# Performance work log

Measured on AMD Instinct MI355X. Metric: run time of the kernel, lower is better.

## Reference

```python
import jax, jax.numpy as jnp
import numpy as np

N = 100000   # num nodes
E = 1600000  # num edges
F = 64       # node_feature_dim
H = 128      # hidden_dim
G = 64       # num graphs in batch
L = 3        # num_gnn_layers


def setup_inputs() -> dict:
    key = jax.random.key(0)
    ks = jax.random.split(key, 24)
    s = 0.05
    nrm = lambda k, shape: jax.random.normal(k, shape, jnp.float32) * s
    return dict(
        node_features=jax.random.normal(ks[0], (N, F), jnp.float32),
        edge_index=jax.random.randint(ks[1], (2, E), 0, N, dtype=jnp.int32),
        batch=jnp.sort(jax.random.randint(ks[2], (N,), 0, G, dtype=jnp.int32)),
        enc_w1=nrm(ks[3], (F, H)), enc_b1=jnp.zeros((H,), jnp.float32),
        enc_w2=nrm(ks[4], (H, H)), enc_b2=jnp.zeros((H,), jnp.float32),
        gcn_w=nrm(ks[5], (L, H, H)), gcn_b=jnp.zeros((L, H), jnp.float32),
        dec_w1=nrm(ks[6], (2 * H, H)), dec_b1=jnp.zeros((H,), jnp.float32),
        dec_w2=nrm(ks[7], (H, 64)), dec_b2=jnp.zeros((64,), jnp.float32),
        dec_w3=nrm(ks[8], (64, 3)), dec_b3=jnp.zeros((3,), jnp.float32),
        val_w1=nrm(ks[9], (2 * H, H)), val_b1=jnp.zeros((H,), jnp.float32),
        val_w2=nrm(ks[10], (H, 1)), val_b2=jnp.zeros((1,), jnp.float32),
    )


def _forward(node_features, edge_index, batch,
             enc_w1, enc_b1, enc_w2, enc_b2, gcn_w, gcn_b,
             dec_w1, dec_b1, dec_w2, dec_b2, dec_w3, dec_b3,
             val_w1, val_b1, val_w2, val_b2):
    n = node_features.shape[0]
    # node encoder (dropout is identity in eval)
    x = jax.nn.relu(node_features @ enc_w1 + enc_b1)
    x = x @ enc_w2 + enc_b2

    # GCN normalization with self-loops (PyG gcn_norm)
    loops = jnp.arange(n, dtype=edge_index.dtype)
    src = jnp.concatenate([edge_index[0], loops])
    dst = jnp.concatenate([edge_index[1], loops])
    deg = jax.ops.segment_sum(jnp.ones_like(src, jnp.float32), dst, num_segments=n)
    dinv = jax.lax.rsqrt(deg)  # deg >= 1 due to self-loops
    norm = (dinv[src] * dinv[dst])[:, None]  # [E+N, 1]

    for l in range(gcn_w.shape[0]):
        xw = x @ gcn_w[l]                      # [N, H]
        msg = xw[src] * norm                   # gather + scale
        agg = jax.ops.segment_sum(msg, dst, num_segments=n) + gcn_b[l]
        x = x + jax.nn.relu(agg)               # residual

    # global pools per graph
    graph_sum = jax.ops.segment_sum(x, batch, num_segments=G)
    counts = jax.ops.segment_sum(jnp.ones((n, 1), x.dtype), batch, num_segments=G)
    graph_mean = graph_sum / jnp.maximum(counts, 1.0)
    graph_max = jax.ops.segment_max(x, batch, num_segments=G)
    graph_repr = jnp.concatenate([graph_mean, graph_max], axis=1)  # [G, 2H]

    h = jax.nn.relu(graph_repr @ dec_w1 + dec_b1)
    h = jax.nn.relu(h @ dec_w2 + dec_b2)
    logits = h @ dec_w3 + dec_b3               # [G, 3]

    adaptation_prob = jax.nn.sigmoid(logits[:, 0])
    layer_priorities = jax.nn.softmax(logits[:, 1:2], axis=-1)
    urgency_score = jax.nn.sigmoid(logits[:, 2])

    v = jax.nn.relu(graph_repr @ val_w1 + val_b1)
    value_estimate = v @ val_w2 + val_b2       # [G, 1]
    return adaptation_prob, layer_priorities, urgency_score, value_estimate


def reference(node_features, edge_index, batch,
              enc_w1, enc_b1, enc_w2, enc_b2, gcn_w, gcn_b,
              dec_w1, dec_b1, dec_w2, dec_b2, dec_w3, dec_b3,
              val_w1, val_b1, val_w2, val_b2):
    return _forward(node_features, edge_index, batch,
                    enc_w1, enc_b1, enc_w2, enc_b2, gcn_w, gcn_b,
                    dec_w1, dec_b1, dec_w2, dec_b2, dec_w3, dec_b3,
                    val_w1, val_b1, val_w2, val_b2)
```

## Files before the change

### kernel.cpp

```cpp
#include <hip/hip_runtime.h>
#include <math.h>

constexpr int HD = 128;
constexpr int FD = 64;
constexpr int PCH = 32;
constexpr int BKT_SHIFT = 8;
constexpr int EPB = 2048;
constexpr float FP8_SCALE = 16.f;
constexpr float FP8_INV_SCALE = 1.f / 16.f;

typedef unsigned int uint;
typedef unsigned short ushort;
typedef unsigned char uchar;

using bf16x8 = __attribute__((ext_vector_type(8))) short;
using f32x4  = __attribute__((ext_vector_type(4))) float;

#if defined(__has_builtin)
#if __has_builtin(__builtin_amdgcn_cvt_pk_f32_fp8) && __has_builtin(__builtin_amdgcn_cvt_pk_fp8_f32)
#define HW_FP8 1
#endif
#endif

static __device__ inline ushort f2bf(float f) {
  uint u = __float_as_uint(f);
  return (ushort)((u + 0x7fffu + ((u >> 16) & 1u)) >> 16);
}
static __device__ inline float bf2f(ushort b) {
  return __uint_as_float((uint)b << 16);
}
static __device__ inline uint pack2bf(float a, float b) {
  return (uint)f2bf(a) | ((uint)f2bf(b) << 16);
}

static __device__ inline uchar enc_fp8_byte(float f) {
#ifdef HW_FP8
  return (uchar)(__builtin_amdgcn_cvt_pk_fp8_f32(f, f, 0, false) & 0xff);
#else
  float a = fabsf(f);
  uint s = (f < 0.f) ? 0x80u : 0u;
  if (!(a > 0.f)) return (uchar)s;
  a = fminf(a, 448.f);
  uint b = __float_as_uint(a);
  int e = (int)(b >> 23) - 127;
  if (e < -6) {
    int q = (int)rintf(a * 512.f);
    if (q <= 0) return (uchar)s;
    if (q >= 8) return (uchar)(s | 0x08u);
    return (uchar)(s | (uint)q);
  }
  uint r = b + 0x7ffffu + ((b >> 20) & 1u);
  uint m = (r >> 20) & 7u;
  int ee = (int)(r >> 23) - 127 + 7;
  if (ee <= 0) return (uchar)(s | 0x08u);
  if (ee > 15) return (uchar)(s | 0x7eu);
  return (uchar)(s | ((uint)ee << 3) | m);
#endif
}

static __device__ inline float dec_fp8_byte(uint em_s) {
  uint s = (em_s & 0x80u) << 24;
  uint em = em_s & 0x7fu;
  float v;
  if (em < 8) v = (float)em * (1.f / 512.f);
  else v = __uint_as_float((em + (120u << 3)) << 20);
  return __uint_as_float(__float_as_uint(v) | s);
}

static __device__ inline void dec_fp8x4(uint u, float* dst) {
#ifdef HW_FP8
  auto a = __builtin_amdgcn_cvt_pk_f32_fp8((int)u, false);
  auto b = __builtin_amdgcn_cvt_pk_f32_fp8((int)u, true);
  dst[0] = a[0]; dst[1] = a[1]; dst[2] = b[0]; dst[3] = b[1];
#else
  dst[0] = dec_fp8_byte(u & 0xffu);
  dst[1] = dec_fp8_byte((u >> 8) & 0xffu);
  dst[2] = dec_fp8_byte((u >> 16) & 0xffu);
  dst[3] = dec_fp8_byte(u >> 24);
#endif
}

__global__ void zero_int_kernel(int* __restrict__ p, int n) {
  int i = blockIdx.x * blockDim.x + threadIdx.x;
  if (i < n) p[i] = 0;
}

__global__ __launch_bounds__(256) void bucket_count_kernel(const int* __restrict__ dst,
    int* __restrict__ bucket_count, int e, int nbk) {
  __shared__ int hist[512];
  int t = threadIdx.x;
  for (int i = t; i < nbk; i += 256) hist[i] = 0;
  __syncthreads();
  int lo = blockIdx.x * EPB;
  int hi = lo + EPB; if (hi > e) hi = e;
  for (int i = lo + t; i < hi; i += 256) atomicAdd(&hist[dst[i] >> BKT_SHIFT], 1);
  __syncthreads();
  for (int i = t; i < nbk; i += 256) {
    int c = hist[i];
    if (c) atomicAdd(&bucket_count[i], c);
  }
}

__global__ __launch_bounds__(512) void bucket_scan_kernel(const int* __restrict__ bucket_count,
    int* __restrict__ bucket_base, int* __restrict__ bucket_cursor, int nbk) {
  __shared__ int sh[512];
  int t = threadIdx.x;
  int v = (t < nbk) ? bucket_count[t] : 0;
  sh[t] = v;
  __syncthreads();
  for (int d = 1; d < 512; d <<= 1) {
    int u = (t >= d) ? sh[t - d] : 0;
    __syncthreads();
    sh[t] += u;
    __syncthreads();
  }
  if (t < nbk) {
    int ex = sh[t] - v;
    bucket_base[t] = ex;
    bucket_cursor[t] = ex;
  }
  if (t == 511) bucket_base[nbk] = sh[511];
}

__global__ __launch_bounds__(256) void bucket_fill_kernel(const int* __restrict__ src,
    const int* __restrict__ dst, int* __restrict__ bucket_cursor,
    uint* __restrict__ pairs, int e, int nbk) {
  __shared__ int hist[512];
  int t = threadIdx.x;
  for (int i = t; i < nbk; i += 256) hist[i] = 0;
  __syncthreads();
  int lo = blockIdx.x * EPB;
  int hi = lo + EPB; if (hi > e) hi = e;
  for (int i = lo + t; i < hi; i += 256) atomicAdd(&hist[dst[i] >> BKT_SHIFT], 1);
  __syncthreads();
  for (int i = t; i < nbk; i += 256) {
    int c = hist[i];
    hist[i] = c ? atomicAdd(&bucket_cursor[i], c) : 0;
  }
  __syncthreads();
  for (int i = lo + t; i < hi; i += 256) {
    int s = src[i], d = dst[i];
    int pos = atomicAdd(&hist[d >> BKT_SHIFT], 1);
    pairs[pos] = ((uint)s << 8) | (uint)(d & 255);
  }
}

__global__ __launch_bounds__(256) void bucket_scatter_kernel(const uint* __restrict__ pairs,
    const int* __restrict__ bucket_base, int* __restrict__ offs,
    float* __restrict__ dinv, int* __restrict__ csr_src, int n, int nbk) {
  __shared__ int cnt[256];
  __shared__ int pre[256];
  int b = blockIdx.x, t = threadIdx.x;
  int node0 = b << BKT_SHIFT;
  bool valid_node = (node0 + t) < n;
  cnt[t] = 0;
  __syncthreads();
  int lo = bucket_base[b], hi = bucket_base[b + 1];
  for (int i = lo + t; i < hi; i += 256)
    atomicAdd(&cnt[pairs[i] & 255u], 1);
  __syncthreads();
  int v = cnt[t];
  pre[t] = v;
  __syncthreads();
  for (int d = 1; d < 256; d <<= 1) {
    int u = (t >= d) ? pre[t - d] : 0;
    __syncthreads();
    pre[t] += u;
    __syncthreads();
  }
  int off = lo + pre[t] - v;
  if (valid_node) {
    offs[node0 + t] = off;
    dinv[node0 + t] = rsqrtf((float)(v + 1));
  }
  __syncthreads();
  cnt[t] = off;
  __syncthreads();
  for (int i = lo + t; i < hi; i += 256) {
    uint pp = pairs[i];
    int pos = atomicAdd(&cnt[pp & 255u], 1);
    csr_src[pos] = (int)(pp >> 8);
  }
  if (b == 0 && t == 0) offs[n] = bucket_base[nbk];
}

__global__ void convert_all_wt_kernel(const float* __restrict__ enc_w1,
    const float* __restrict__ enc_w2, const float* __restrict__ gcn_w,
    ushort* __restrict__ wt_e1, ushort* __restrict__ wt_e2, ushort* __restrict__ wt_g,
    int L) {
  const int S0 = 128 * FD, S1 = 128 * HD;
  int i = blockIdx.x * 256 + threadIdx.x;
  if (i < S0) {
    int c = i / FD, k = i - c * FD;
    wt_e1[i] = f2bf(enc_w1[k * 128 + c]);
  } else if (i < S0 + S1) {
    int j = i - S0;
    int c = j / HD, k = j - c * HD;
    wt_e2[j] = f2bf(enc_w2[k * 128 + c]);
  } else if (i < S0 + S1 + L * S1) {
    int j = i - S0 - S1;
    int l = j / S1, jj = j - l * S1;
    int c = jj / HD, k = jj - c * HD;
    wt_g[(size_t)l * S1 + jj] = f2bf(gcn_w[(size_t)l * HD * HD + k * 128 + c]);
  }
}

template<typename TA, int K, bool BIAS, bool RELU, bool FP8OUT>
__global__ __launch_bounds__(256) void mfma_gemm_kernel(const TA* __restrict__ A,
    const ushort* __restrict__ Wt, const float* __restrict__ bias,
    void* __restrict__ Cout, const float* __restrict__ dinv, int M) {
  __shared__ ushort As[64 * K];
  __shared__ ushort Ws[128 * K];
  const int tid = threadIdx.x;
  const int r0 = blockIdx.x * 64;

  if constexpr (sizeof(TA) == 4) {
    constexpr int C4 = K / 4;
    const float4* A4 = (const float4*)A;
    #pragma unroll
    for (int i = tid; i < 64 * C4; i += 256) {
      int r = i / C4, c4 = i - r * C4;
      int row = r0 + r;
      float4 v = make_float4(0.f, 0.f, 0.f, 0.f);
      if (row < M) v = A4[(size_t)row * C4 + c4];
      ushort4 u;
      u.x = f2bf(v.x); u.y = f2bf(v.y); u.z = f2bf(v.z); u.w = f2bf(v.w);
      int elem = (r * K + c4 * 4) ^ ((r & 7) << 3);
      *(ushort4*)&As[elem] = u;
    }
  } else {
    constexpr int C8 = K / 8;
    const uint4* A4 = (const uint4*)A;
    #pragma unroll
    for (int i = tid; i < 64 * C8; i += 256) {
      int r = i / C8, c8 = i - r * C8;
      int row = r0 + r;
      uint4 v = make_uint4(0u, 0u, 0u, 0u);
      if (row < M) v = A4[(size_t)row * C8 + c8];
      int elem = (r * K + c8 * 8) ^ ((r & 7) << 3);
      *(uint4*)&As[elem] = v;
    }
  }
  {
    constexpr int C8 = K / 8;
    const uint4* W4 = (const uint4*)Wt;
    #pragma unroll
    for (int i = tid; i < 128 * C8; i += 256) {
      int c = i / C8, k8 = i - c * C8;
      uint4 v = W4[i];
      int elem = (c * K + k8 * 8) ^ ((c & 7) << 3);
      *(uint4*)&Ws[elem] = v;
    }
  }
  __syncthreads();

  const int l = tid & 63;
  const int wid = tid >> 6;
  const int lr = l & 15;
  const int lk = l >> 4;
  const int wr = wid * 16;
  f32x4 acc[8];
  #pragma unroll
  for (int cb = 0; cb < 8; ++cb) acc[cb] = (f32x4){0.f, 0.f, 0.f, 0.f};

  #pragma unroll
  for (int kc = 0; kc < K / 32; ++kc) {
    int ar = wr + lr;
    bf16x8 af = *(const bf16x8*)&As[(ar * K + kc * 32 + lk * 8) ^ ((ar & 7) << 3)];
    #pragma unroll
    for (int cb = 0; cb < 8; ++cb) {
      int col = cb * 16 + lr;
      bf16x8 bfr = *(const bf16x8*)&Ws[(col * K + kc * 32 + lk * 8) ^ ((col & 7) << 3)];
      acc[cb] = __builtin_amdgcn_mfma_f32_16x16x32_bf16(af, bfr, acc[cb], 0, 0, 0);
    }
  }

  if constexpr (FP8OUT) {
    uchar* C8p = (uchar*)Cout;
    float dv[4];
    #pragma unroll
    for (int j = 0; j < 4; ++j) {
      int row = r0 + wr + lk * 4 + j;
      dv[j] = (row < M) ? dinv[row] * FP8_SCALE : 0.f;
    }
    #pragma unroll
    for (int cb = 0; cb < 8; ++cb) {
      int col = cb * 16 + lr;
      #pragma unroll
      for (int j = 0; j < 4; ++j) {
        int row = r0 + wr + lk * 4 + j;
        if (row < M) {
          C8p[(size_t)row * 128 + col] = enc_fp8_byte(acc[cb][j] * dv[j]);
        }
      }
    }
  } else {
    ushort* Cb = (ushort*)Cout;
    #pragma unroll
    for (int cb = 0; cb < 8; ++cb) {
      int col = cb * 16 + lr;
      float bb = BIAS ? bias[col] : 0.f;
      #pragma unroll
      for (int j = 0; j < 4; ++j) {
        int row = r0 + wr + lk * 4 + j;
        if (row < M) {
          float o = acc[cb][j] + bb;
          if (RELU) o = fmaxf(o, 0.f);
          Cb[(size_t)row * 128 + col] = f2bf(o);
        }
      }
    }
  }
}

__global__ __launch_bounds__(256) void agg_update_kernel(
    const uchar* __restrict__ xws, ushort* __restrict__ x,
    const int* __restrict__ csr_src, const int* __restrict__ offs,
    const float* __restrict__ dinv, const float* __restrict__ bias, int n) {
  int node = blockIdx.x * 4 + (threadIdx.x >> 6);
  if (node >= n) return;
  int lane = threadIdx.x & 63;
  int grp = lane >> 4;
  int cl = lane & 15;
  const uint2* xw2 = (const uint2*)xws;
  float acc[8];
  #pragma unroll
  for (int k = 0; k < 8; ++k) acc[k] = 0.f;

  auto add_row = [&](uint2 v) {
    float f[4];
    dec_fp8x4(v.x, f);
    acc[0] += f[0]; acc[1] += f[1]; acc[2] += f[2]; acc[3] += f[3];
    dec_fp8x4(v.y, f);
    acc[4] += f[0]; acc[5] += f[1]; acc[6] += f[2]; acc[7] += f[3];
  };

  int beg = offs[node], end = offs[node + 1];
  int j = beg + grp;
  for (; j + 12 < end; j += 16) {
    int s0 = csr_src[j];
    int s1 = csr_src[j + 4];
    int s2 = csr_src[j + 8];
    int s3 = csr_src[j + 12];
    uint2 v0 = xw2[(size_t)s0 * 16 + cl];
    uint2 v1 = xw2[(size_t)s1 * 16 + cl];
    uint2 v2 = xw2[(size_t)s2 * 16 + cl];
    uint2 v3 = xw2[(size_t)s3 * 16 + cl];
    add_row(v0); add_row(v1); add_row(v2); add_row(v3);
  }
  for (; j + 4 < end; j += 8) {
    int s0 = csr_src[j];
    int s1 = csr_src[j + 4];
    uint2 v0 = xw2[(size_t)s0 * 16 + cl];
    uint2 v1 = xw2[(size_t)s1 * 16 + cl];
    add_row(v0); add_row(v1);
  }
  if (j < end) {
    uint2 v0 = xw2[(size_t)csr_src[j] * 16 + cl];
    add_row(v0);
  }
  if (grp == 0) {
    uint2 vi = xw2[(size_t)node * 16 + cl];
    add_row(vi);
  }
  #pragma unroll
  for (int k = 0; k < 8; ++k) {
    acc[k] += __shfl_xor(acc[k], 16);
    acc[k] += __shfl_xor(acc[k], 32);
  }
  if (grp == 0) {
    float di = dinv[node] * FP8_INV_SCALE;
    const float4* b4 = (const float4*)bias;
    float4 bb0 = b4[cl * 2], bb1 = b4[cl * 2 + 1];
    float bbv[8] = {bb0.x, bb0.y, bb0.z, bb0.w, bb1.x, bb1.y, bb1.z, bb1.w};
    uint4* xv4 = (uint4*)x;
    size_t xi = (size_t)node * 16 + cl;
    uint4 xv = xv4[xi];
    uint xu[4] = {xv.x, xv.y, xv.z, xv.w};
    float o[8];
    #pragma unroll
    for (int q = 0; q < 4; ++q) {
      float lo = __uint_as_float(xu[q] << 16);
      float hi = __uint_as_float(xu[q] & 0xffff0000u);
      o[2 * q]     = fmaxf(fmaf(acc[2 * q],     di, bbv[2 * q]),     0.f) + lo;
      o[2 * q + 1] = fmaxf(fmaf(acc[2 * q + 1], di, bbv[2 * q + 1]), 0.f) + hi;
    }
    uint4 ou;
    ou.x = pack2bf(o[0], o[1]);
    ou.y = pack2bf(o[2], o[3]);
    ou.z = pack2bf(o[4], o[5]);
    ou.w = pack2bf(o[6], o[7]);
    xv4[xi] = ou;
  }
}

__global__ void bounds_kernel(const int* __restrict__ batch, int* __restrict__ startg,
                              int n, int ng) {
  int i = blockIdx.x * blockDim.x + threadIdx.x;
  if (i > n) return;
  int bi = (i < n) ? batch[i] : ng;
  int bp = (i == 0) ? -1 : batch[i - 1];
  for (int g = bp + 1; g <= bi && g <= ng; ++g) startg[g] = i;
}

__global__ __launch_bounds__(256) void pool_partial_kernel(const ushort* __restrict__ x,
    const int* __restrict__ startg, float* __restrict__ psum, float* __restrict__ pmax) {
  __shared__ float ssum[16][128];
  __shared__ float smax[16][128];
  int g = blockIdx.x / PCH, ch = blockIdx.x % PCH;
  int t = threadIdx.x;
  int rg = t >> 4, cg = t & 15;
  int s0 = startg[g], s1 = startg[g + 1];
  int cnt = s1 - s0;
  int len = (cnt + PCH - 1) / PCH;
  int lo = s0 + ch * len;
  int hi = lo + len; if (hi > s1) hi = s1;
  float sum[8], mx[8];
  #pragma unroll
  for (int k = 0; k < 8; ++k) { sum[k] = 0.f; mx[k] = -INFINITY; }
  const uint4* x4 = (const uint4*)x;
  for (int r = lo + rg; r < hi; r += 16) {
    uint4 v = x4[(size_t)r * 16 + cg];
    uint uu[4] = {v.x, v.y, v.z, v.w};
    #pragma unroll
    for (int q = 0; q < 4; ++q) {
      float a = __uint_as_float(uu[q] << 16);
      float b = __uint_as_float(uu[q] & 0xffff0000u);
      sum[2 * q] += a;     mx[2 * q]     = fmaxf(mx[2 * q], a);
      sum[2 * q + 1] += b; mx[2 * q + 1] = fmaxf(mx[2 * q + 1], b);
    }
  }
  #pragma unroll
  for (int k = 0; k < 8; ++k) {
    ssum[rg][cg * 8 + k] = sum[k];
    smax[rg][cg * 8 + k] = mx[k];
  }
  __syncthreads();
  #pragma unroll
  for (int d = 8; d > 0; d >>= 1) {
    if (rg < d) {
      #pragma unroll
      for (int k = 0; k < 8; ++k) {
        int c = cg * 8 + k;
        ssum[rg][c] += ssum[rg + d][c];
        smax[rg][c] = fmaxf(smax[rg][c], smax[rg + d][c]);
      }
    }
    __syncthreads();
  }
  if (rg == 0) {
    #pragma unroll
    for (int k = 0; k < 8; ++k) {
      int c = cg * 8 + k;
      psum[(size_t)blockIdx.x * HD + c] = ssum[0][c];
      pmax[(size_t)blockIdx.x * HD + c] = smax[0][c];
    }
  }
}

__global__ __launch_bounds__(128) void heads_kernel(
    const float* __restrict__ psum, const float* __restrict__ pmax,
    const int* __restrict__ startg,
    const float* __restrict__ dw1, const float* __restrict__ db1,
    const float* __restrict__ dw2, const float* __restrict__ db2,
    const float* __restrict__ dw3, const float* __restrict__ db3,
    const float* __restrict__ vw1, const float* __restrict__ vb1,
    const float* __restrict__ vw2, const float* __restrict__ vb2,
    float* __restrict__ out, int ng) {
  __shared__ float rep[256];
  __shared__ float h1[128];
  __shared__ float h2[64];
  __shared__ float v1[128];
  int g = blockIdx.x, t = threadIdx.x;
  {
    float sum = 0.f, mx = -INFINITY;
    #pragma unroll
    for (int ch = 0; ch < PCH; ++ch) {
      sum += psum[(size_t)(g * PCH + ch) * HD + t];
      mx = fmaxf(mx, pmax[(size_t)(g * PCH + ch) * HD + t]);
    }
    int cnt = startg[g + 1] - startg[g];
    float denom = (float)(cnt > 0 ? cnt : 1);
    rep[t] = sum / denom;
    rep[128 + t] = mx;
  }
  __syncthreads();
  float a = db1[t], b = vb1[t];
  for (int k = 0; k < 256; ++k) {
    float rv = rep[k];
    a = fmaf(rv, dw1[k * 128 + t], a);
    b = fmaf(rv, vw1[k * 128 + t], b);
  }
  h1[t] = fmaxf(a, 0.f);
  v1[t] = fmaxf(b, 0.f);
  __syncthreads();
  if (t < 64) {
    float c = db2[t];
    for (int k = 0; k < 128; ++k) c = fmaf(h1[k], dw2[k * 64 + t], c);
    h2[t] = fmaxf(c, 0.f);
  }
  __syncthreads();
  if (t == 0) {
    float l0 = db3[0], l2 = db3[2];
    for (int k = 0; k < 64; ++k) {
      l0 = fmaf(h2[k], dw3[k * 3 + 0], l0);
      l2 = fmaf(h2[k], dw3[k * 3 + 2], l2);
    }
    out[g] = 1.f / (1.f + expf(-l0));
    out[ng + g] = 1.0f;
    out[2 * ng + g] = 1.f / (1.f + expf(-l2));
    float v = vb2[0];
    for (int k = 0; k < 128; ++k) v = fmaf(v1[k], vw2[k], v);
    out[3 * ng + g] = v;
  }
}

extern "C" void kernel_launch(void* const* d_in, const int* in_sizes, int n_in,
                              void* d_out, int out_size, void* d_ws, size_t ws_size,
                              hipStream_t stream) {
  const float* nf     = (const float*)d_in[0];
  const int*   ei     = (const int*)d_in[1];
  const int*   batch  = (const int*)d_in[2];
  const float* enc_w1 = (const float*)d_in[3];
  const float* enc_b1 = (const float*)d_in[4];
  const float* enc_w2 = (const float*)d_in[5];
  const float* enc_b2 = (const float*)d_in[6];
  const float* gcn_w  = (const float*)d_in[7];
  const float* gcn_b  = (const float*)d_in[8];
  const float* dec_w1 = (const float*)d_in[9];
  const float* dec_b1 = (const float*)d_in[10];
  const float* dec_w2 = (const float*)d_in[11];
  const float* dec_b2 = (const float*)d_in[12];
  const float* dec_w3 = (const float*)d_in[13];
  const float* dec_b3 = (const float*)d_in[14];
  const float* val_w1 = (const float*)d_in[15];
  const float* val_b1 = (const float*)d_in[16];
  const float* val_w2 = (const float*)d_in[17];
  const float* val_b2 = (const float*)d_in[18];
  float* out = (float*)d_out;

  const int n = in_sizes[0] / FD;
  const int e = in_sizes[1] / 2;
  const int L = in_sizes[7] / (HD * HD);
  const int G = out_size / 4;

  char* p = (char*)d_ws;
  auto carve = [&](size_t bytes) {
    void* r = (void*)p;
    p += (bytes + 255) & ~(size_t)255;
    return r;
  };
  ushort* x       = (ushort*)carve((size_t)n * HD * 2);
  ushort* xwb     = (ushort*)carve((size_t)n * HD * 2);
  uchar*  xw8     = (uchar*)carve((size_t)n * HD);
  float*  dinv    = (float*)carve((size_t)n * 4);
  int*    offs    = (int*)carve((size_t)(n + 1) * 4);
  int*    csr_src = (int*)carve((size_t)e * 4);
  int*    startg  = (int*)carve((size_t)(G + 1) * 4);
  float*  psum    = (float*)carve((size_t)G * PCH * HD * 4);
  float*  pmax    = (float*)carve((size_t)G * PCH * HD * 4);
  const int nbk   = (n + (1 << BKT_SHIFT) - 1) >> BKT_SHIFT;
  int*    bucket_count  = (int*)carve((size_t)nbk * 4);
  int*    bucket_base   = (int*)carve((size_t)(nbk + 1) * 4);
  int*    bucket_cursor = (int*)carve((size_t)nbk * 4);
  ushort* wt_e1   = (ushort*)carve((size_t)128 * FD * 2);
  ushort* wt_e2   = (ushort*)carve((size_t)128 * HD * 2);
  ushort* wt_g    = (ushort*)carve((size_t)3 * 128 * HD * 2);
  uint*   pairs   = (uint*)xwb;

  const int gemm_grid = (n + 63) / 64;
  const int ebk_grid = (e + EPB - 1) / EPB;

  zero_int_kernel<<<(nbk + 255) / 256, 256, 0, stream>>>(bucket_count, nbk);
  bucket_count_kernel<<<ebk_grid, 256, 0, stream>>>(ei + e, bucket_count, e, nbk);
  bucket_scan_kernel<<<1, 512, 0, stream>>>(bucket_count, bucket_base, bucket_cursor, nbk);
  bucket_fill_kernel<<<ebk_grid, 256, 0, stream>>>(ei, ei + e, bucket_cursor, pairs, e, nbk);
  bucket_scatter_kernel<<<nbk, 256, 0, stream>>>(pairs, bucket_base, offs, dinv, csr_src, n, nbk);

  {
    int tot = 128 * FD + 128 * HD + L * 128 * HD;
    convert_all_wt_kernel<<<(tot + 255) / 256, 256, 0, stream>>>(
        enc_w1, enc_w2, gcn_w, wt_e1, wt_e2, wt_g, L);
  }

  mfma_gemm_kernel<float, FD, true, true, false><<<gemm_grid, 256, 0, stream>>>(
      nf, wt_e1, enc_b1, xwb, nullptr, n);
  mfma_gemm_kernel<ushort, HD, true, false, false><<<gemm_grid, 256, 0, stream>>>(
      xwb, wt_e2, enc_b2, x, nullptr, n);

  for (int l = 0; l < L; ++l) {
    mfma_gemm_kernel<ushort, HD, false, false, true><<<gemm_grid, 256, 0, stream>>>(
        x, wt_g + (size_t)l * 128 * HD, nullptr, xw8, dinv, n);
    agg_update_kernel<<<(n + 3) / 4, 256, 0, stream>>>(
        xw8, x, csr_src, offs, dinv, gcn_b + (size_t)l * HD, n);
  }

  bounds_kernel<<<(n + 1 + 255) / 256, 256, 0, stream>>>(batch, startg, n, G);
  pool_partial_kernel<<<G * PCH, 256, 0, stream>>>(x, startg, psum, pmax);
  heads_kernel<<<G, 128, 0, stream>>>(psum, pmax, startg,
      dec_w1, dec_b1, dec_w2, dec_b2, dec_w3, dec_b3,
      val_w1, val_b1, val_w2, val_b2, out, G);
}
```

Measured before the change: 373.6 us.

## Fuse encoder GEMMs via shared memory and make GCN GEMM persistent

The two encoder GEMMs are merged into one kernel that keeps the ReLU intermediate in LDS, so the bf16 hidden tensor is never written to or re-read from global memory. The per-layer GCN GEMM becomes a persistent grid-stride kernel with 768 blocks that loads the weight tile into LDS once per block and reuses it across row tiles. The pairs buffer gets its own allocation because the aliased intermediate buffer is gone. The fused encoder uses more LDS per block (about 80KB), which may lower occupancy.

```diff
diff --git a/kernel.cpp b/kernel.cpp
--- a/kernel.cpp
+++ b/kernel.cpp
@@ -205,18 +205,20 @@
   }
 }
 
-template<typename TA, int K, bool BIAS, bool RELU, bool FP8OUT>
-__global__ __launch_bounds__(256) void mfma_gemm_kernel(const TA* __restrict__ A,
-    const ushort* __restrict__ Wt, const float* __restrict__ bias,
-    void* __restrict__ Cout, const float* __restrict__ dinv, int M) {
-  __shared__ ushort As[64 * K];
-  __shared__ ushort Ws[128 * K];
+__global__ __launch_bounds__(256) void encoder_fused_kernel(
+    const float* __restrict__ nf, const ushort* __restrict__ wt1,
+    const float* __restrict__ b1, const ushort* __restrict__ wt2,
+    const float* __restrict__ b2, ushort* __restrict__ xout, int M) {
+  __shared__ ushort As[64 * FD];
+  __shared__ ushort W1s[128 * FD];
+  __shared__ ushort Mid[64 * HD];
+  __shared__ ushort W2s[128 * HD];
   const int tid = threadIdx.x;
   const int r0 = blockIdx.x * 64;
 
-  if constexpr (sizeof(TA) == 4) {
-    constexpr int C4 = K / 4;
-    const float4* A4 = (const float4*)A;
+  {
+    constexpr int C4 = FD / 4;
+    const float4* A4 = (const float4*)nf;
     #pragma unroll
     for (int i = tid; i < 64 * C4; i += 256) {
       int r = i / C4, c4 = i - r * C4;
@@ -225,31 +227,30 @@
       if (row < M) v = A4[(size_t)row * C4 + c4];
       ushort4 u;
       u.x = f2bf(v.x); u.y = f2bf(v.y); u.z = f2bf(v.z); u.w = f2bf(v.w);
-      int elem = (r * K + c4 * 4) ^ ((r & 7) << 3);
+      int elem = (r * FD + c4 * 4) ^ ((r & 7) << 3);
       *(ushort4*)&As[elem] = u;
     }
-  } else {
-    constexpr int C8 = K / 8;
-    const uint4* A4 = (const uint4*)A;
-    #pragma unroll
-    for (int i = tid; i < 64 * C8; i += 256) {
-      int r = i / C8, c8 = i - r * C8;
-      int row = r0 + r;
-      uint4 v = make_uint4(0u, 0u, 0u, 0u);
-      if (row < M) v = A4[(size_t)row * C8 + c8];
-      int elem = (r * K + c8 * 8) ^ ((r & 7) << 3);
-      *(uint4*)&As[elem] = v;
-    }
-  }
-  {
-    constexpr int C8 = K / 8;
-    const uint4* W4 = (const uint4*)Wt;
+  }
+  {
+    constexpr int C8 = FD / 8;
+    const uint4* W4 = (const uint4*)wt1;
     #pragma unroll
     for (int i = tid; i < 128 * C8; i += 256) {
       int c = i / C8, k8 = i - c * C8;
       uint4 v = W4[i];
-      int elem = (c * K + k8 * 8) ^ ((c & 7) << 3);
-      *(uint4*)&Ws[elem] = v;
+      int elem = (c * FD + k8 * 8) ^ ((c & 7) << 3);
+      *(uint4*)&W1s[elem] = v;
+    }
+  }
+  {
+    constexpr int C8 = HD / 8;
+    const uint4* W4 = (const uint4*)wt2;
+    #pragma unroll
+    for (int i = tid; i < 128 * C8; i += 256) {
+      int c = i / C8, k8 = i - c * C8;
+      uint4 v = W4[i];
+      int elem = (c * HD + k8 * 8) ^ ((c & 7) << 3);
+      *(uint4*)&W2s[elem] = v;
     }
   }
   __syncthreads();
@@ -259,24 +260,122 @@
   const int lr = l & 15;
   const int lk = l >> 4;
   const int wr = wid * 16;
-  f32x4 acc[8];
-  #pragma unroll
-  for (int cb = 0; cb < 8; ++cb) acc[cb] = (f32x4){0.f, 0.f, 0.f, 0.f};
-
-  #pragma unroll
-  for (int kc = 0; kc < K / 32; ++kc) {
-    int ar = wr + lr;
-    bf16x8 af = *(const bf16x8*)&As[(ar * K + kc * 32 + lk * 8) ^ ((ar & 7) << 3)];
+
+  {
+    f32x4 acc[8];
+    #pragma unroll
+    for (int cb = 0; cb < 8; ++cb) acc[cb] = (f32x4){0.f, 0.f, 0.f, 0.f};
+    #pragma unroll
+    for (int kc = 0; kc < FD / 32; ++kc) {
+      int ar = wr + lr;
+      bf16x8 af = *(const bf16x8*)&As[(ar * FD + kc * 32 + lk * 8) ^ ((ar & 7) << 3)];
+      #pragma unroll
+      for (int cb = 0; cb < 8; ++cb) {
+        int col = cb * 16 + lr;
+        bf16x8 bfr = *(const bf16x8*)&W1s[(col * FD + kc * 32 + lk * 8) ^ ((col & 7) << 3)];
+        acc[cb] = __builtin_amdgcn_mfma_f32_16x16x32_bf16(af, bfr, acc[cb], 0, 0, 0);
+      }
+    }
     #pragma unroll
     for (int cb = 0; cb < 8; ++cb) {
       int col = cb * 16 + lr;
-      bf16x8 bfr = *(const bf16x8*)&Ws[(col * K + kc * 32 + lk * 8) ^ ((col & 7) << 3)];
-      acc[cb] = __builtin_amdgcn_mfma_f32_16x16x32_bf16(af, bfr, acc[cb], 0, 0, 0);
-    }
-  }
-
-  if constexpr (FP8OUT) {
-    uchar* C8p = (uchar*)Cout;
+      float bb = b1[col];
+      #pragma unroll
+      for (int j = 0; j < 4; ++j) {
+        int row = wr + lk * 4 + j;
+        float o = fmaxf(acc[cb][j] + bb, 0.f);
+        Mid[(row * HD + col) ^ ((row & 7) << 3)] = f2bf(o);
+      }
+    }
+  }
+  __syncthreads();
+
+  {
+    f32x4 acc[8];
+    #pragma unroll
+    for (int cb = 0; cb < 8; ++cb) acc[cb] = (f32x4){0.f, 0.f, 0.f, 0.f};
+    #pragma unroll
+    for (int kc = 0; kc < HD / 32; ++kc) {
+      int ar = wr + lr;
+      bf16x8 af = *(const bf16x8*)&Mid[(ar * HD + kc * 32 + lk * 8) ^ ((ar & 7) << 3)];
+      #pragma unroll
+      for (int cb = 0; cb < 8; ++cb) {
+        int col = cb * 16 + lr;
+        bf16x8 bfr = *(const bf16x8*)&W2s[(col * HD + kc * 32 + lk * 8) ^ ((col & 7) << 3)];
+        acc[cb] = __builtin_amdgcn_mfma_f32_16x16x32_bf16(af, bfr, acc[cb], 0, 0, 0);
+      }
+    }
+    #pragma unroll
+    for (int cb = 0; cb < 8; ++cb) {
+      int col = cb * 16 + lr;
+      float bb = b2[col];
+      #pragma unroll
+      for (int j = 0; j < 4; ++j) {
+        int row = r0 + wr + lk * 4 + j;
+        if (row < M) xout[(size_t)row * 128 + col] = f2bf(acc[cb][j] + bb);
+      }
+    }
+  }
+}
+
+__global__ __launch_bounds__(256) void mfma_gemm_fp8_kernel(const ushort* __restrict__ A,
+    const ushort* __restrict__ Wt, uchar* __restrict__ Cout,
+    const float* __restrict__ dinv, int M, int ntiles) {
+  __shared__ ushort As[64 * HD];
+  __shared__ ushort Ws[128 * HD];
+  const int tid = threadIdx.x;
+
+  {
+    constexpr int C8 = HD / 8;
+    const uint4* W4 = (const uint4*)Wt;
+    #pragma unroll
+    for (int i = tid; i < 128 * C8; i += 256) {
+      int c = i / C8, k8 = i - c * C8;
+      uint4 v = W4[i];
+      int elem = (c * HD + k8 * 8) ^ ((c & 7) << 3);
+      *(uint4*)&Ws[elem] = v;
+    }
+  }
+
+  const int l = tid & 63;
+  const int wid = tid >> 6;
+  const int lr = l & 15;
+  const int lk = l >> 4;
+  const int wr = wid * 16;
+
+  for (int tile = blockIdx.x; tile < ntiles; tile += gridDim.x) {
+    __syncthreads();
+    const int r0 = tile * 64;
+    {
+      constexpr int C8 = HD / 8;
+      const uint4* A4 = (const uint4*)A;
+      #pragma unroll
+      for (int i = tid; i < 64 * C8; i += 256) {
+        int r = i / C8, c8 = i - r * C8;
+        int row = r0 + r;
+        uint4 v = make_uint4(0u, 0u, 0u, 0u);
+        if (row < M) v = A4[(size_t)row * C8 + c8];
+        int elem = (r * HD + c8 * 8) ^ ((r & 7) << 3);
+        *(uint4*)&As[elem] = v;
+      }
+    }
+    __syncthreads();
+
+    f32x4 acc[8];
+    #pragma unroll
+    for (int cb = 0; cb < 8; ++cb) acc[cb] = (f32x4){0.f, 0.f, 0.f, 0.f};
+    #pragma unroll
+    for (int kc = 0; kc < HD / 32; ++kc) {
+      int ar = wr + lr;
+      bf16x8 af = *(const bf16x8*)&As[(ar * HD + kc * 32 + lk * 8) ^ ((ar & 7) << 3)];
+      #pragma unroll
+      for (int cb = 0; cb < 8; ++cb) {
+        int col = cb * 16 + lr;
+        bf16x8 bfr = *(const bf16x8*)&Ws[(col * HD + kc * 32 + lk * 8) ^ ((col & 7) << 3)];
+        acc[cb] = __builtin_amdgcn_mfma_f32_16x16x32_bf16(af, bfr, acc[cb], 0, 0, 0);
+      }
+    }
+
     float dv[4];
     #pragma unroll
     for (int j = 0; j < 4; ++j) {
@@ -290,23 +389,7 @@
       for (int j = 0; j < 4; ++j) {
         int row = r0 + wr + lk * 4 + j;
         if (row < M) {
-          C8p[(size_t)row * 128 + col] = enc_fp8_byte(acc[cb][j] * dv[j]);
-        }
-      }
-    }
-  } else {
-    ushort* Cb = (ushort*)Cout;
-    #pragma unroll
-    for (int cb = 0; cb < 8; ++cb) {
-      int col = cb * 16 + lr;
-      float bb = BIAS ? bias[col] : 0.f;
-      #pragma unroll
-      for (int j = 0; j < 4; ++j) {
-        int row = r0 + wr + lk * 4 + j;
-        if (row < M) {
-          float o = acc[cb][j] + bb;
-          if (RELU) o = fmaxf(o, 0.f);
-          Cb[(size_t)row * 128 + col] = f2bf(o);
+          Cout[(size_t)row * 128 + col] = enc_fp8_byte(acc[cb][j] * dv[j]);
         }
       }
     }
@@ -551,8 +634,8 @@
     return r;
   };
   ushort* x       = (ushort*)carve((size_t)n * HD * 2);
-  ushort* xwb     = (ushort*)carve((size_t)n * HD * 2);
   uchar*  xw8     = (uchar*)carve((size_t)n * HD);
+  uint*   pairs   = (uint*)carve((size_t)e * 4);
   float*  dinv    = (float*)carve((size_t)n * 4);
   int*    offs    = (int*)carve((size_t)(n + 1) * 4);
   int*    csr_src = (int*)carve((size_t)e * 4);
@@ -566,10 +649,10 @@
   ushort* wt_e1   = (ushort*)carve((size_t)128 * FD * 2);
   ushort* wt_e2   = (ushort*)carve((size_t)128 * HD * 2);
   ushort* wt_g    = (ushort*)carve((size_t)3 * 128 * HD * 2);
-  uint*   pairs   = (uint*)xwb;
-
-  const int gemm_grid = (n + 63) / 64;
+
+  const int ntiles = (n + 63) / 64;
   const int ebk_grid = (e + EPB - 1) / EPB;
+  const int gemm_grid = 768;
 
   zero_int_kernel<<<(nbk + 255) / 256, 256, 0, stream>>>(bucket_count, nbk);
   bucket_count_kernel<<<ebk_grid, 256, 0, stream>>>(ei + e, bucket_count, e, nbk);
@@ -583,14 +666,12 @@
         enc_w1, enc_w2, gcn_w, wt_e1, wt_e2, wt_g, L);
   }
 
-  mfma_gemm_kernel<float, FD, true, true, false><<<gemm_grid, 256, 0, stream>>>(
-      nf, wt_e1, enc_b1, xwb, nullptr, n);
-  mfma_gemm_kernel<ushort, HD, true, false, false><<<gemm_grid, 256, 0, stream>>>(
-      xwb, wt_e2, enc_b2, x, nullptr, n);
+  encoder_fused_kernel<<<ntiles, 256, 0, stream>>>(
+      nf, wt_e1, enc_b1, wt_e2, enc_b2, x, n);
 
   for (int l = 0; l < L; ++l) {
-    mfma_gemm_kernel<ushort, HD, false, false, true><<<gemm_grid, 256, 0, stream>>>(
-        x, wt_g + (size_t)l * 128 * HD, nullptr, xw8, dinv, n);
+    mfma_gemm_fp8_kernel<<<gemm_grid, 256, 0, stream>>>(
+        x, wt_g + (size_t)l * 128 * HD, xw8, dinv, n, ntiles);
     agg_update_kernel<<<(n + 3) / 4, 256, 0, stream>>>(
         xw8, x, csr_src, offs, dinv, gcn_b + (size_t)l * HD, n);
   }
```

New measurement: 359.9 us. 3.7% less time.
